# Performance work log

Measured on AMD Instinct MI355X. Metric: run time of the kernel, lower is better.

The kernel has to match this reference:

```python
import jax, jax.numpy as jnp
import numpy as np

N_NODES = 50000
N_EDGES = 500000  # directed; reverse pairs (2i, 2i+1)
NODE_DIM = 160
BOND_DIM = 14
HIDDEN = 160
DEPTH = 3


def setup_inputs() -> dict:
    key = jax.random.key(0)
    ks = jax.random.split(key, 10)
    x = jax.random.normal(ks[0], (N_NODES, NODE_DIM), dtype=jnp.float32)
    edge_attr = jax.random.normal(ks[1], (N_EDGES, BOND_DIM), dtype=jnp.float32)
    # build undirected edges materialized in both directions (chemprop style)
    half = N_EDGES // 2
    u = jax.random.randint(ks[2], (half,), 0, N_NODES)
    v = jax.random.randint(ks[3], (half,), 0, N_NODES)
    src = jnp.stack([u, v], axis=1).reshape(-1)  # [E]
    dst = jnp.stack([v, u], axis=1).reshape(-1)  # [E]
    edge_index = jnp.stack([src, dst], axis=0).astype(jnp.int64)
    rev_edge_index = (jnp.arange(N_EDGES) ^ 1).astype(jnp.int64)
    s = 0.05
    Wi_w = jax.random.normal(ks[4], (HIDDEN, NODE_DIM + BOND_DIM), dtype=jnp.float32) * s
    Wi_b = jnp.zeros((HIDDEN,), dtype=jnp.float32)
    Wh_w = jax.random.normal(ks[5], (HIDDEN, HIDDEN), dtype=jnp.float32) * s
    Wh_b = jnp.zeros((HIDDEN,), dtype=jnp.float32)
    Wo_w = jax.random.normal(ks[6], (HIDDEN, NODE_DIM + HIDDEN), dtype=jnp.float32) * s
    Wo_b = jnp.zeros((HIDDEN,), dtype=jnp.float32)
    return {"x": x, "edge_attr": edge_attr, "edge_index": edge_index,
            "rev_edge_index": rev_edge_index, "Wi_w": Wi_w, "Wi_b": Wi_b,
            "Wh_w": Wh_w, "Wh_b": Wh_b, "Wo_w": Wo_w, "Wo_b": Wo_b}


def reference(x, edge_attr, edge_index, rev_edge_index, Wi_w, Wi_b, Wh_w, Wh_b, Wo_w, Wo_b):
    # BondMessagePassing.forward (eval mode: dropout = identity)
    src, dst = edge_index[0], edge_index[1]
    n_nodes = x.shape[0]
    # H_0 = relu(W_i([x_src ; edge_attr]))            [E, H]
    H0 = jax.nn.relu(jnp.concatenate([x[src], edge_attr], axis=1) @ Wi_w.T + Wi_b)
    H = H0
    for _ in range(1, DEPTH):
        # message: scatter-sum over dst, gather at src, subtract reverse edge
        Magg = jax.ops.segment_sum(H, dst, num_segments=n_nodes)  # [N, H]
        M = Magg[src] - H[rev_edge_index]                          # [E, H]
        # update: relu(H_0 + W_h(M))
        H = jax.nn.relu(H0 + M @ Wh_w.T + Wh_b)
    M = jax.ops.segment_sum(H, dst, num_segments=n_nodes)          # [N, H]
    M = jnp.where(jnp.sum(M, axis=1, keepdims=True) == 0, x, M)
    out = jax.nn.relu(jnp.concatenate([x, M], axis=1) @ Wo_w.T + Wo_b)  # [N, H]
    return out
```

## Files before the change

### kernel.cpp

```cpp
#include <hip/hip_runtime.h>


#define E_EDGES 500000
#define N_NODES 50000
#define HD      160
#define BD      14
#define K1      174
#define KO      320

#define TE 64
#define KC 16
#define NC2 (HD / KC)
#define WP  (HD + 8)

#define TM   128
#define WHP  164
#define WIEP 20

typedef __attribute__((ext_vector_type(4))) short v4s;
typedef __attribute__((ext_vector_type(4))) float v4f;

__device__ __forceinline__ unsigned short f2b(float v) {
    unsigned u = __float_as_uint(v);
    u += 0x7FFFu + ((u >> 16) & 1u);
    return (unsigned short)(u >> 16);
}
__device__ __forceinline__ float b2f(unsigned short h) {
    return __uint_as_float(((unsigned)h) << 16);
}

__device__ __forceinline__ v4s mdiff(ushort4 s, ushort4 r) {
    v4s a;
    a[0] = (short)f2b(b2f(s.x) - b2f(r.x));
    a[1] = (short)f2b(b2f(s.y) - b2f(r.y));
    a[2] = (short)f2b(b2f(s.z) - b2f(r.z));
    a[3] = (short)f2b(b2f(s.w) - b2f(r.w));
    return a;
}

__global__ void k_zero(float* __restrict__ p, long n)
{
    const long i = (long)blockIdx.x * 1024 + (long)threadIdx.x * 4;
    if (i + 3 < n) *(float4*)(p + i) = make_float4(0.f, 0.f, 0.f, 0.f);
}

__device__ __forceinline__
void gemm_chunk(float acc[4][10], const float At[KC][TE + 4],
                const float Wt[KC][WP], int tr, int tc)
{
    #pragma unroll
    for (int k = 0; k < KC; ++k) {
        const float4 a  = *(const float4*)&At[k][tr * 4];
        const float* wp = &Wt[k][tc * 10];
        float w[10];
        #pragma unroll
        for (int j = 0; j < 10; j += 2) {
            const float2 w2 = *(const float2*)(wp + j);
            w[j] = w2.x; w[j + 1] = w2.y;
        }
        #pragma unroll
        for (int j = 0; j < 10; ++j) {
            acc[0][j] = fmaf(a.x, w[j], acc[0][j]);
            acc[1][j] = fmaf(a.y, w[j], acc[1][j]);
            acc[2][j] = fmaf(a.z, w[j], acc[2][j]);
            acc[3][j] = fmaf(a.w, w[j], acc[3][j]);
        }
    }
}

__global__ void k_csr_count(const int* __restrict__ dst, int* __restrict__ cnt)
{
    const int e = blockIdx.x * 256 + threadIdx.x;
    if (e < E_EDGES) atomicAdd(&cnt[dst[e]], 1);
}

#define BPT 49
__global__ __launch_bounds__(1024)
void k_csr_scan(const int* __restrict__ cnt, int* __restrict__ ptr)
{
    __shared__ int part[1024];
    const int t  = threadIdx.x;
    const int lo = t * BPT;
    const int hi = min(lo + BPT, N_NODES);
    int s = 0;
    for (int i = lo; i < hi; ++i) s += cnt[i];
    part[t] = s;
    __syncthreads();
    for (int off = 1; off < 1024; off <<= 1) {
        int v = 0;
        if (t >= off) v = part[t - off];
        __syncthreads();
        if (t >= off) part[t] += v;
        __syncthreads();
    }
    int run = (t == 0) ? 0 : part[t - 1];
    for (int i = lo; i < hi; ++i) { ptr[i] = run; run += cnt[i]; }
    if (t == 1023) ptr[N_NODES] = part[1023];
}

__global__ void k_csr_fill(const int* __restrict__ dst, const int* __restrict__ ptr,
                           int* __restrict__ cur, int* __restrict__ eid)
{
    const int e = blockIdx.x * 256 + threadIdx.x;
    if (e < E_EDGES) {
        const int d   = dst[e];
        const int pos = atomicAdd(&cur[d], 1);
        eid[ptr[d] + pos] = e;
    }
}

__global__ __launch_bounds__(256, 2)
void k_nodeproj(const float* __restrict__ x, const float* __restrict__ Wi,
                const float* __restrict__ bi, unsigned short* __restrict__ Pb)
{
    __shared__ float At[KC][TE + 4];
    __shared__ float Wt[KC][WP];

    const int  t    = threadIdx.x;
    const long base = (long)blockIdx.x * TE;
    const int  se  = t >> 2;
    const int  skq = t & 3;
    const long gn  = base + se;
    const long gnc = (gn < N_NODES) ? gn : 0;
    const float* xrow = x + gnc * HD;
    const int tr = t >> 4, tc = t & 15;

    float acc[4][10];
    #pragma unroll
    for (int i = 0; i < 4; ++i)
        #pragma unroll
        for (int j = 0; j < 10; ++j) acc[i][j] = 0.f;

    for (int c = 0; c < NC2; ++c) {
        const int k0 = c * KC;
        __syncthreads();
        {
            const float4 v = *(const float4*)(xrow + k0 + skq * 4);
            At[skq * 4 + 0][se] = v.x;
            At[skq * 4 + 1][se] = v.y;
            At[skq * 4 + 2][se] = v.z;
            At[skq * 4 + 3][se] = v.w;
        }
        for (int i = t; i < HD * KC; i += 256) {
            const int kk = i & (KC - 1);
            const int h  = i >> 4;
            Wt[kk][h] = Wi[h * K1 + k0 + kk];
        }
        __syncthreads();
        gemm_chunk(acc, At, Wt, tr, tc);
    }
    #pragma unroll
    for (int i = 0; i < 4; ++i) {
        const long n = base + tr * 4 + i;
        if (n >= N_NODES) break;
        unsigned short* pp = Pb + n * HD + tc * 10;
        #pragma unroll
        for (int j = 0; j < 10; j += 2) {
            const float v0 = acc[i][j]     + bi[tc * 10 + j];
            const float v1 = acc[i][j + 1] + bi[tc * 10 + j + 1];
            *(ushort2*)(pp + j) = make_ushort2(f2b(v0), f2b(v1));
        }
    }
}

__global__ __launch_bounds__(256, 3)
void k_h0b_p(const float* __restrict__ ea, const int* __restrict__ src,
             const float* __restrict__ Wi, const unsigned short* __restrict__ Pb,
             unsigned short* __restrict__ Hb)
{
    __shared__ float At[KC][TE + 4];
    __shared__ float Wt[KC][WP];

    const int  t    = threadIdx.x;
    const long base = (long)blockIdx.x * TE;
    const int  se  = t >> 2;
    const int  skq = t & 3;
    const long ge  = base + se;
    const long gec = (ge < E_EDGES) ? ge : 0;
    const float* erow = ea + gec * BD;
    const int wk = t & 15, wh0 = t >> 4;
    const int tr = t >> 4, tc = t & 15;

    int es[4];
    #pragma unroll
    for (int i = 0; i < 4; ++i) {
        const long e = base + tr * 4 + i;
        es[i] = (e < E_EDGES) ? src[e] : 0;
    }

    #pragma unroll
    for (int j = 0; j < 4; ++j) {
        const int k = skq * 4 + j;
        At[k][se] = (k < BD) ? erow[k] : 0.f;
    }
    #pragma unroll
    for (int m = 0; m < 10; ++m)
        Wt[wk][wh0 + 16 * m] = (wk < BD) ? Wi[(wh0 + 16 * m) * K1 + HD + wk] : 0.f;

    ushort2 praw[4][5];
    #pragma unroll
    for (int i = 0; i < 4; ++i) {
        const unsigned short* prow = Pb + (long)es[i] * HD + tc * 10;
        #pragma unroll
        for (int q = 0; q < 5; ++q) praw[i][q] = *(const ushort2*)(prow + 2 * q);
    }

    __syncthreads();
    float acc[4][10];
    #pragma unroll
    for (int i = 0; i < 4; ++i)
        #pragma unroll
        for (int j = 0; j < 10; ++j) acc[i][j] = 0.f;
    gemm_chunk(acc, At, Wt, tr, tc);

    #pragma unroll
    for (int i = 0; i < 4; ++i) {
        const long e = base + tr * 4 + i;
        if (e >= E_EDGES) break;
        unsigned short* hp = Hb + e * HD + tc * 10;
        #pragma unroll
        for (int j = 0; j < 10; j += 2) {
            float v0 = acc[i][j]     + b2f(praw[i][j / 2].x);
            float v1 = acc[i][j + 1] + b2f(praw[i][j / 2].y);
            v0 = v0 > 0.f ? v0 : 0.f;
            v1 = v1 > 0.f ? v1 : 0.f;
            *(ushort2*)(hp + j) = make_ushort2(f2b(v0), f2b(v1));
        }
    }
}

template <int FINAL>
__global__ void k_segb(const unsigned short* __restrict__ Hb,
                       const int* __restrict__ ptr, const int* __restrict__ eid,
                       const float* __restrict__ x,
                       unsigned short* __restrict__ Sb, float* __restrict__ S)
{
    const int  lane = threadIdx.x & 63;
    const int  w    = threadIdx.x >> 6;
    const long n    = (long)blockIdx.x * 4 + w;
    if (n >= N_NODES) return;
    const int p0 = ptr[n], p1 = ptr[n + 1];
    float a0 = 0.f, a1 = 0.f, a2 = 0.f;
    for (int i = p0; i < p1; ++i) {
        const unsigned short* row = Hb + (long)eid[i] * HD;
        a0 += b2f(row[lane]);
        a1 += b2f(row[64 + lane]);
        if (lane < 32) a2 += b2f(row[128 + lane]);
    }
    const long sb = n * HD;
    if (FINAL) {
        float s = a0 + a1 + a2;
        #pragma unroll
        for (int off = 32; off > 0; off >>= 1) s += __shfl_xor(s, off, 64);
        if (s == 0.f) {
            S[sb + lane]      = x[sb + lane];
            S[sb + 64 + lane] = x[sb + 64 + lane];
            if (lane < 32) S[sb + 128 + lane] = x[sb + 128 + lane];
            return;
        }
        S[sb + lane]      = a0;
        S[sb + 64 + lane] = a1;
        if (lane < 32) S[sb + 128 + lane] = a2;
    } else {
        Sb[sb + lane]      = f2b(a0);
        Sb[sb + 64 + lane] = f2b(a1);
        if (lane < 32) Sb[sb + 128 + lane] = f2b(a2);
    }
}

__global__ __launch_bounds__(512, 6)
void k_updm1(const unsigned short* __restrict__ Sb,
             const int* __restrict__ src,
             const float* __restrict__ Wh, const float* __restrict__ bh,
             unsigned short* __restrict__ Hb)
{
    __shared__ unsigned short Whl[HD * WHP];

    const int t = threadIdx.x;
    for (int i = t * 4; i < HD * HD; i += 2048) {
        const int h = i / HD, k = i % HD;
        const float4 wv = *(const float4*)(Wh + h * HD + k);
        *(ushort4*)&Whl[h * WHP + k] =
            make_ushort4(f2b(wv.x), f2b(wv.y), f2b(wv.z), f2b(wv.w));
    }
    __syncthreads();

    const int  w    = t >> 6;
    const int  lane = t & 63;
    const int  cl   = lane & 15;
    const int  kq   = lane >> 4;
    const long base = (long)blockIdx.x * TM + w * 16;

    const long eA  = base + cl;
    const long eAs = (eA < E_EDGES) ? eA : 0;
    const int  sA  = src[eAs];
    const unsigned short* sbrow = Sb + (long)sA * HD + kq * 4;
    const unsigned short* rvrow = Hb + (eAs ^ 1) * HD + kq * 4;

    v4f acc[10];
    #pragma unroll
    for (int n = 0; n < 10; ++n) acc[n] = (v4f){0.f, 0.f, 0.f, 0.f};

    ushort4 ps = *(const ushort4*)(sbrow);
    ushort4 pr = *(const ushort4*)(rvrow);
    #pragma unroll
    for (int c = 0; c < 10; ++c) {
        const v4s a = mdiff(ps, pr);
        if (c < 9) {
            ps = *(const ushort4*)(sbrow + (c + 1) * KC);
            pr = *(const ushort4*)(rvrow + (c + 1) * KC);
        }
        #pragma unroll
        for (int n = 0; n < 10; ++n) {
            const v4s b = *(const v4s*)&Whl[(n * 16 + cl) * WHP + c * KC + kq * 4];
            acc[n] = __builtin_amdgcn_mfma_f32_16x16x16bf16_1k(a, b, acc[n], 0, 0, 0);
        }
    }

    #pragma unroll
    for (int n = 0; n < 10; ++n) {
        const int col = n * 16 + cl;
        const float bb = bh[col];
        #pragma unroll
        for (int rr = 0; rr < 4; ++rr) {
            const long e = base + kq * 4 + rr;
            if (e < E_EDGES) {
                unsigned short* hp = Hb + e * HD + col;
                float v = b2f(*hp) + acc[n][rr] + bb;
                v = v > 0.f ? v : 0.f;
                *hp = f2b(v);
            }
        }
    }
}

__global__ __launch_bounds__(512, 4)
void k_updm2(const unsigned short* __restrict__ Sb,
             const float* __restrict__ ea, const int* __restrict__ src,
             const float* __restrict__ Wi, const float* __restrict__ Wh,
             const float* __restrict__ bh,
             const unsigned short* __restrict__ Pb,
             unsigned short* __restrict__ Hb)
{
    __shared__ unsigned short Whl[HD * WHP];
    __shared__ unsigned short Wie[HD * WIEP];

    const int t = threadIdx.x;
    for (int i = t * 4; i < HD * HD; i += 2048) {
        const int h = i / HD, k = i % HD;
        const float4 wv = *(const float4*)(Wh + h * HD + k);
        *(ushort4*)&Whl[h * WHP + k] =
            make_ushort4(f2b(wv.x), f2b(wv.y), f2b(wv.z), f2b(wv.w));
    }
    if (t < HD) {
        const float* wr = Wi + (long)t * K1 + HD;
        #pragma unroll
        for (int k = 0; k < BD; ++k) Wie[t * WIEP + k] = f2b(wr[k]);
        Wie[t * WIEP + 14] = 0;
        Wie[t * WIEP + 15] = 0;
    }
    __syncthreads();

    const int  w    = t >> 6;
    const int  lane = t & 63;
    const int  cl   = lane & 15;
    const int  kq   = lane >> 4;
    const long base = (long)blockIdx.x * TM + w * 16;

    const long eA  = base + cl;
    const long eAs = (eA < E_EDGES) ? eA : 0;
    const int  sA  = src[eAs];
    const unsigned short* sbrow = Sb + (long)sA * HD + kq * 4;
    const unsigned short* rvrow = Hb + (eAs ^ 1) * HD + kq * 4;

    v4s aq;
    {
        const float* earow = ea + eAs * BD;
        #pragma unroll
        for (int j = 0; j < 4; ++j) {
            const int k = kq * 4 + j;
            aq[j] = (short)((k < BD) ? f2b(earow[k]) : 0);
        }
    }
    int srcC[4];
    #pragma unroll
    for (int rr = 0; rr < 4; ++rr) {
        const long e = base + kq * 4 + rr;
        srcC[rr] = src[(e < E_EDGES) ? e : 0];
    }

    float h0[10][4];
    #pragma unroll
    for (int n = 0; n < 10; ++n) {
        const v4s bq = *(const v4s*)&Wie[(n * 16 + cl) * WIEP + kq * 4];
        v4f q = __builtin_amdgcn_mfma_f32_16x16x16bf16_1k(
                    aq, bq, (v4f){0.f, 0.f, 0.f, 0.f}, 0, 0, 0);
        const int col = n * 16 + cl;
        #pragma unroll
        for (int rr = 0; rr < 4; ++rr) {
            const float pv = b2f(Pb[(long)srcC[rr] * HD + col]);
            const float v  = pv + q[rr];
            h0[n][rr] = v > 0.f ? v : 0.f;
        }
    }

    v4f acc[10];
    #pragma unroll
    for (int n = 0; n < 10; ++n) acc[n] = (v4f){0.f, 0.f, 0.f, 0.f};

    ushort4 ps = *(const ushort4*)(sbrow);
    ushort4 pr = *(const ushort4*)(rvrow);
    #pragma unroll
    for (int c = 0; c < 10; ++c) {
        const v4s a = mdiff(ps, pr);
        if (c < 9) {
            ps = *(const ushort4*)(sbrow + (c + 1) * KC);
            pr = *(const ushort4*)(rvrow + (c + 1) * KC);
        }
        #pragma unroll
        for (int n = 0; n < 10; ++n) {
            const v4s b = *(const v4s*)&Whl[(n * 16 + cl) * WHP + c * KC + kq * 4];
            acc[n] = __builtin_amdgcn_mfma_f32_16x16x16bf16_1k(a, b, acc[n], 0, 0, 0);
        }
    }

    #pragma unroll
    for (int n = 0; n < 10; ++n) {
        const int col = n * 16 + cl;
        const float bb = bh[col];
        #pragma unroll
        for (int rr = 0; rr < 4; ++rr) {
            const long e = base + kq * 4 + rr;
            if (e < E_EDGES) {
                float v = h0[n][rr] + acc[n][rr] + bb;
                v = v > 0.f ? v : 0.f;
                Hb[e * HD + col] = f2b(v);
            }
        }
    }
}

__global__ __launch_bounds__(256, 2)
void k_out(const float* __restrict__ x, const float* __restrict__ Mg,
           const float* __restrict__ Wo, const float* __restrict__ bo,
           float* __restrict__ out)
{
    __shared__ float At[KC][TE + 4];
    __shared__ float Wt[KC][WP];

    const int  t    = threadIdx.x;
    const long base = (long)blockIdx.x * TE;
    const int  se  = t >> 2;
    const int  skq = t & 3;
    const long gn  = base + se;
    const bool ev  = gn < N_NODES;
    const long gnc = ev ? gn : 0;
    const float* xrow = x  + gnc * HD;
    const float* mrow = Mg + gnc * HD;
    const int tr = t >> 4, tc = t & 15;

    float acc[4][10];
    #pragma unroll
    for (int i = 0; i < 4; ++i)
        #pragma unroll
        for (int j = 0; j < 10; ++j) acc[i][j] = 0.f;

    for (int c = 0; c < KO / KC; ++c) {
        const int k0 = c * KC;
        __syncthreads();
        {
            const int kb = k0 + skq * 4;
            const float4 v = (kb < HD) ? *(const float4*)(xrow + kb)
                                       : *(const float4*)(mrow + (kb - HD));
            At[skq * 4 + 0][se] = v.x;
            At[skq * 4 + 1][se] = v.y;
            At[skq * 4 + 2][se] = v.z;
            At[skq * 4 + 3][se] = v.w;
        }
        for (int i = t; i < HD * KC; i += 256) {
            const int kk = i & (KC - 1);
            const int h  = i >> 4;
            Wt[kk][h] = Wo[h * KO + k0 + kk];
        }
        __syncthreads();
        gemm_chunk(acc, At, Wt, tr, tc);
    }
    #pragma unroll
    for (int i = 0; i < 4; ++i) {
        const long n = base + tr * 4 + i;
        if (n >= N_NODES) break;
        float* op = out + n * HD + tc * 10;
        #pragma unroll
        for (int j = 0; j < 10; j += 2) {
            float v0 = acc[i][j]     + bo[tc * 10 + j];
            float v1 = acc[i][j + 1] + bo[tc * 10 + j + 1];
            v0 = v0 > 0.f ? v0 : 0.f;
            v1 = v1 > 0.f ? v1 : 0.f;
            *(float2*)(op + j) = make_float2(v0, v1);
        }
    }
}

extern "C" void kernel_launch(void* const* d_in, const int* in_sizes, int n_in,
                              void* d_out, int out_size, void* d_ws, size_t ws_size,
                              hipStream_t stream)
{
    const float* x  = (const float*)d_in[0];
    const float* ea = (const float*)d_in[1];
    const int*   ei = (const int*)d_in[2];
    const float* Wi = (const float*)d_in[4];
    const float* bi = (const float*)d_in[5];
    const float* Wh = (const float*)d_in[6];
    const float* bh = (const float*)d_in[7];
    const float* Wo = (const float*)d_in[8];
    const float* bo = (const float*)d_in[9];
    float* out = (float*)d_out;

    const int* src = ei;
    const int* dst = ei + E_EDGES;

    const int gE  = (E_EDGES + TE - 1) / TE;
    const int gM  = (E_EDGES + TM - 1) / TM;
    const int gN  = (N_NODES + TE - 1) / TE;
    const int gF  = (N_NODES + 3) / 4;
    const int gEe = (E_EDGES + 255) / 256;

    char* w = (char*)d_ws;
    unsigned short* Hb = (unsigned short*)(w);
    float* Mf  = (float*)(w + 160000000);
    int*   ptr = (int*)  (w + 192000000);
    int*   cnt = (int*)  (w + 192200016);
    int*   cur = (int*)  (w + 192400016);
    int*   eid = (int*)  (w + 192600016);
    unsigned short* Pb = (unsigned short*)d_out;
    unsigned short* Sb = (unsigned short*)((char*)d_out + 16000000);

    k_zero<<<(100000 + 1023) / 1024, 256, 0, stream>>>((float*)cnt, 100000);
    k_csr_count<<<gEe, 256, 0, stream>>>(dst, cnt);
    k_csr_scan<<<1, 1024, 0, stream>>>(cnt, ptr);
    k_csr_fill<<<gEe, 256, 0, stream>>>(dst, ptr, cur, eid);

    k_nodeproj<<<gN, 256, 0, stream>>>(x, Wi, bi, Pb);
    k_h0b_p<<<gE, 256, 0, stream>>>(ea, src, Wi, Pb, Hb);
    k_segb<0><<<gF, 256, 0, stream>>>(Hb, ptr, eid, x, Sb, nullptr);
    k_updm1<<<gM, 512, 0, stream>>>(Sb, src, Wh, bh, Hb);
    k_segb<0><<<gF, 256, 0, stream>>>(Hb, ptr, eid, x, Sb, nullptr);
    k_updm2<<<gM, 512, 0, stream>>>(Sb, ea, src, Wi, Wh, bh, Pb, Hb);
    k_segb<1><<<gF, 256, 0, stream>>>(Hb, ptr, eid, x, nullptr, Mf);
    k_out<<<gN, 256, 0, stream>>>(x, Mf, Wo, bo, out);
}
```

Before: 1.073 ms.

## Use MFMA for initial edge projection, unroll segment sums, deepen prefetch

Replaces the FP32 shared-memory GEMM kernel for H0 with an MFMA-based kernel that reads bond weights straight from global memory, with no LDS staging. The segment-sum loop is unrolled by two with separate accumulators to raise memory-level parallelism on the gathers. The update kernels prefetch two K-chunks ahead instead of one. k_updm2 drops its LDS copy of the bond weights and raises its launch-bounds occupancy target. The trade-offs are more register pressure and redundant global weight loads, plus per-column scalar scattered stores in the new H0 kernel.

Result: slower. 1.579 ms (+47.2%).

```diff
diff --git a/kernel.cpp b/kernel.cpp
--- a/kernel.cpp
+++ b/kernel.cpp
@@ -15,7 +15,6 @@
 
 #define TM   128
 #define WHP  164
-#define WIEP 20
 
 typedef __attribute__((ext_vector_type(4))) short v4s;
 typedef __attribute__((ext_vector_type(4))) float v4f;
@@ -163,68 +162,66 @@
     }
 }
 
-__global__ __launch_bounds__(256, 3)
-void k_h0b_p(const float* __restrict__ ea, const int* __restrict__ src,
-             const float* __restrict__ Wi, const unsigned short* __restrict__ Pb,
-             unsigned short* __restrict__ Hb)
-{
-    __shared__ float At[KC][TE + 4];
-    __shared__ float Wt[KC][WP];
-
+__global__ __launch_bounds__(512, 6)
+void k_h0m(const float* __restrict__ ea, const int* __restrict__ src,
+           const float* __restrict__ Wi, const unsigned short* __restrict__ Pb,
+           unsigned short* __restrict__ Hb)
+{
     const int  t    = threadIdx.x;
-    const long base = (long)blockIdx.x * TE;
-    const int  se  = t >> 2;
-    const int  skq = t & 3;
-    const long ge  = base + se;
-    const long gec = (ge < E_EDGES) ? ge : 0;
-    const float* erow = ea + gec * BD;
-    const int wk = t & 15, wh0 = t >> 4;
-    const int tr = t >> 4, tc = t & 15;
-
-    int es[4];
-    #pragma unroll
-    for (int i = 0; i < 4; ++i) {
-        const long e = base + tr * 4 + i;
-        es[i] = (e < E_EDGES) ? src[e] : 0;
-    }
-
-    #pragma unroll
-    for (int j = 0; j < 4; ++j) {
-        const int k = skq * 4 + j;
-        At[k][se] = (k < BD) ? erow[k] : 0.f;
-    }
-    #pragma unroll
-    for (int m = 0; m < 10; ++m)
-        Wt[wk][wh0 + 16 * m] = (wk < BD) ? Wi[(wh0 + 16 * m) * K1 + HD + wk] : 0.f;
-
-    ushort2 praw[4][5];
-    #pragma unroll
-    for (int i = 0; i < 4; ++i) {
-        const unsigned short* prow = Pb + (long)es[i] * HD + tc * 10;
-        #pragma unroll
-        for (int q = 0; q < 5; ++q) praw[i][q] = *(const ushort2*)(prow + 2 * q);
-    }
-
-    __syncthreads();
-    float acc[4][10];
-    #pragma unroll
-    for (int i = 0; i < 4; ++i)
-        #pragma unroll
-        for (int j = 0; j < 10; ++j) acc[i][j] = 0.f;
-    gemm_chunk(acc, At, Wt, tr, tc);
-
-    #pragma unroll
-    for (int i = 0; i < 4; ++i) {
-        const long e = base + tr * 4 + i;
-        if (e >= E_EDGES) break;
-        unsigned short* hp = Hb + e * HD + tc * 10;
-        #pragma unroll
-        for (int j = 0; j < 10; j += 2) {
-            float v0 = acc[i][j]     + b2f(praw[i][j / 2].x);
-            float v1 = acc[i][j + 1] + b2f(praw[i][j / 2].y);
-            v0 = v0 > 0.f ? v0 : 0.f;
-            v1 = v1 > 0.f ? v1 : 0.f;
-            *(ushort2*)(hp + j) = make_ushort2(f2b(v0), f2b(v1));
+    const int  w    = t >> 6;
+    const int  lane = t & 63;
+    const int  cl   = lane & 15;
+    const int  kq   = lane >> 4;
+    const long base = (long)blockIdx.x * TM + w * 16;
+
+    const long eA  = base + cl;
+    const long eAs = (eA < E_EDGES) ? eA : 0;
+
+    v4s aq;
+    {
+        const float* earow = ea + eAs * BD;
+        if (kq < 3) {
+            #pragma unroll
+            for (int j = 0; j < 4; ++j) aq[j] = (short)f2b(earow[kq * 4 + j]);
+        } else {
+            aq[0] = (short)f2b(earow[12]);
+            aq[1] = (short)f2b(earow[13]);
+            aq[2] = 0; aq[3] = 0;
+        }
+    }
+    int srcC[4];
+    #pragma unroll
+    for (int rr = 0; rr < 4; ++rr) {
+        const long e = base + kq * 4 + rr;
+        srcC[rr] = src[(e < E_EDGES) ? e : 0];
+    }
+
+    #pragma unroll
+    for (int n = 0; n < 10; ++n) {
+        const int col = n * 16 + cl;
+        v4s bq;
+        {
+            const float* wr = Wi + (long)col * K1 + HD + kq * 4;
+            if (kq < 3) {
+                #pragma unroll
+                for (int j = 0; j < 4; ++j) bq[j] = (short)f2b(wr[j]);
+            } else {
+                bq[0] = (short)f2b(wr[0]);
+                bq[1] = (short)f2b(wr[1]);
+                bq[2] = 0; bq[3] = 0;
+            }
+        }
+        const v4f q = __builtin_amdgcn_mfma_f32_16x16x16bf16_1k(
+                          aq, bq, (v4f){0.f, 0.f, 0.f, 0.f}, 0, 0, 0);
+        #pragma unroll
+        for (int rr = 0; rr < 4; ++rr) {
+            const long e = base + kq * 4 + rr;
+            if (e < E_EDGES) {
+                const float pv = b2f(Pb[(long)srcC[rr] * HD + col]);
+                float v = pv + q[rr];
+                v = v > 0.f ? v : 0.f;
+                Hb[e * HD + col] = f2b(v);
+            }
         }
     }
 }
@@ -241,12 +238,29 @@
     if (n >= N_NODES) return;
     const int p0 = ptr[n], p1 = ptr[n + 1];
     float a0 = 0.f, a1 = 0.f, a2 = 0.f;
-    for (int i = p0; i < p1; ++i) {
-        const unsigned short* row = Hb + (long)eid[i] * HD;
-        a0 += b2f(row[lane]);
-        a1 += b2f(row[64 + lane]);
-        if (lane < 32) a2 += b2f(row[128 + lane]);
-    }
+    float c0 = 0.f, c1 = 0.f, c2 = 0.f;
+    int i = p0;
+    for (; i + 2 <= p1; i += 2) {
+        const int e0 = eid[i], e1 = eid[i + 1];
+        const unsigned short* r0 = Hb + (long)e0 * HD;
+        const unsigned short* r1 = Hb + (long)e1 * HD;
+        a0 += b2f(r0[lane]);
+        c0 += b2f(r1[lane]);
+        a1 += b2f(r0[64 + lane]);
+        c1 += b2f(r1[64 + lane]);
+        if (lane < 32) {
+            a2 += b2f(r0[128 + lane]);
+            c2 += b2f(r1[128 + lane]);
+        }
+    }
+    if (i < p1) {
+        const unsigned short* r0 = Hb + (long)eid[i] * HD;
+        a0 += b2f(r0[lane]);
+        a1 += b2f(r0[64 + lane]);
+        if (lane < 32) a2 += b2f(r0[128 + lane]);
+    }
+    a0 += c0; a1 += c1; a2 += c2;
+
     const long sb = n * HD;
     if (FINAL) {
         float s = a0 + a1 + a2;
@@ -301,14 +315,17 @@
     #pragma unroll
     for (int n = 0; n < 10; ++n) acc[n] = (v4f){0.f, 0.f, 0.f, 0.f};
 
-    ushort4 ps = *(const ushort4*)(sbrow);
-    ushort4 pr = *(const ushort4*)(rvrow);
+    ushort4 ps0 = *(const ushort4*)(sbrow);
+    ushort4 pr0 = *(const ushort4*)(rvrow);
+    ushort4 ps1 = *(const ushort4*)(sbrow + KC);
+    ushort4 pr1 = *(const ushort4*)(rvrow + KC);
     #pragma unroll
     for (int c = 0; c < 10; ++c) {
-        const v4s a = mdiff(ps, pr);
-        if (c < 9) {
-            ps = *(const ushort4*)(sbrow + (c + 1) * KC);
-            pr = *(const ushort4*)(rvrow + (c + 1) * KC);
+        const v4s a = mdiff(ps0, pr0);
+        ps0 = ps1; pr0 = pr1;
+        if (c + 2 < 10) {
+            ps1 = *(const ushort4*)(sbrow + (c + 2) * KC);
+            pr1 = *(const ushort4*)(rvrow + (c + 2) * KC);
         }
         #pragma unroll
         for (int n = 0; n < 10; ++n) {
@@ -334,7 +351,7 @@
     }
 }
 
-__global__ __launch_bounds__(512, 4)
+__global__ __launch_bounds__(512, 6)
 void k_updm2(const unsigned short* __restrict__ Sb,
              const float* __restrict__ ea, const int* __restrict__ src,
              const float* __restrict__ Wi, const float* __restrict__ Wh,
@@ -343,7 +360,6 @@
              unsigned short* __restrict__ Hb)
 {
     __shared__ unsigned short Whl[HD * WHP];
-    __shared__ unsigned short Wie[HD * WIEP];
 
     const int t = threadIdx.x;
     for (int i = t * 4; i < HD * HD; i += 2048) {
@@ -352,13 +368,6 @@
         *(ushort4*)&Whl[h * WHP + k] =
             make_ushort4(f2b(wv.x), f2b(wv.y), f2b(wv.z), f2b(wv.w));
     }
-    if (t < HD) {
-        const float* wr = Wi + (long)t * K1 + HD;
-        #pragma unroll
-        for (int k = 0; k < BD; ++k) Wie[t * WIEP + k] = f2b(wr[k]);
-        Wie[t * WIEP + 14] = 0;
-        Wie[t * WIEP + 15] = 0;
-    }
     __syncthreads();
 
     const int  w    = t >> 6;
@@ -376,10 +385,13 @@
     v4s aq;
     {
         const float* earow = ea + eAs * BD;
-        #pragma unroll
-        for (int j = 0; j < 4; ++j) {
-            const int k = kq * 4 + j;
-            aq[j] = (short)((k < BD) ? f2b(earow[k]) : 0);
+        if (kq < 3) {
+            #pragma unroll
+            for (int j = 0; j < 4; ++j) aq[j] = (short)f2b(earow[kq * 4 + j]);
+        } else {
+            aq[0] = (short)f2b(earow[12]);
+            aq[1] = (short)f2b(earow[13]);
+            aq[2] = 0; aq[3] = 0;
         }
     }
     int srcC[4];
@@ -392,10 +404,21 @@
     float h0[10][4];
     #pragma unroll
     for (int n = 0; n < 10; ++n) {
-        const v4s bq = *(const v4s*)&Wie[(n * 16 + cl) * WIEP + kq * 4];
-        v4f q = __builtin_amdgcn_mfma_f32_16x16x16bf16_1k(
-                    aq, bq, (v4f){0.f, 0.f, 0.f, 0.f}, 0, 0, 0);
         const int col = n * 16 + cl;
+        v4s bq;
+        {
+            const float* wr = Wi + (long)col * K1 + HD + kq * 4;
+            if (kq < 3) {
+                #pragma unroll
+                for (int j = 0; j < 4; ++j) bq[j] = (short)f2b(wr[j]);
+            } else {
+                bq[0] = (short)f2b(wr[0]);
+                bq[1] = (short)f2b(wr[1]);
+                bq[2] = 0; bq[3] = 0;
+            }
+        }
+        const v4f q = __builtin_amdgcn_mfma_f32_16x16x16bf16_1k(
+                          aq, bq, (v4f){0.f, 0.f, 0.f, 0.f}, 0, 0, 0);
         #pragma unroll
         for (int rr = 0; rr < 4; ++rr) {
             const float pv = b2f(Pb[(long)srcC[rr] * HD + col]);
@@ -408,14 +431,17 @@
     #pragma unroll
     for (int n = 0; n < 10; ++n) acc[n] = (v4f){0.f, 0.f, 0.f, 0.f};
 
-    ushort4 ps = *(const ushort4*)(sbrow);
-    ushort4 pr = *(const ushort4*)(rvrow);
+    ushort4 ps0 = *(const ushort4*)(sbrow);
+    ushort4 pr0 = *(const ushort4*)(rvrow);
+    ushort4 ps1 = *(const ushort4*)(sbrow + KC);
+    ushort4 pr1 = *(const ushort4*)(rvrow + KC);
     #pragma unroll
     for (int c = 0; c < 10; ++c) {
-        const v4s a = mdiff(ps, pr);
-        if (c < 9) {
-            ps = *(const ushort4*)(sbrow + (c + 1) * KC);
-            pr = *(const ushort4*)(rvrow + (c + 1) * KC);
+        const v4s a = mdiff(ps0, pr0);
+        ps0 = ps1; pr0 = pr1;
+        if (c + 2 < 10) {
+            ps1 = *(const ushort4*)(sbrow + (c + 2) * KC);
+            pr1 = *(const ushort4*)(rvrow + (c + 2) * KC);
         }
         #pragma unroll
         for (int n = 0; n < 10; ++n) {
@@ -519,7 +545,6 @@
     const int* src = ei;
     const int* dst = ei + E_EDGES;
 
-    const int gE  = (E_EDGES + TE - 1) / TE;
     const int gM  = (E_EDGES + TM - 1) / TM;
     const int gN  = (N_NODES + TE - 1) / TE;
     const int gF  = (N_NODES + 3) / 4;
@@ -541,7 +566,7 @@
     k_csr_fill<<<gEe, 256, 0, stream>>>(dst, ptr, cur, eid);
 
     k_nodeproj<<<gN, 256, 0, stream>>>(x, Wi, bi, Pb);
-    k_h0b_p<<<gE, 256, 0, stream>>>(ea, src, Wi, Pb, Hb);
+    k_h0m<<<gM, 512, 0, stream>>>(ea, src, Wi, Pb, Hb);
     k_segb<0><<<gF, 256, 0, stream>>>(Hb, ptr, eid, x, Sb, nullptr);
     k_updm1<<<gM, 512, 0, stream>>>(Sb, src, Wh, bh, Hb);
     k_segb<0><<<gF, 256, 0, stream>>>(Hb, ptr, eid, x, Sb, nullptr);
```
